# Performance work log

Measured on AMD Instinct MI355X. Metric: run time of the kernel, lower is better.

The kernel has to match this reference:

```python
import jax, jax.numpy as jnp
from jax import lax
import numpy as np

P, K1, K2 = 8, 5, 9  # nPaths, small/large ECA kernel sizes (from nDim=1024, nPaths=8)
LN_EPS = 1e-5


def setup_inputs() -> dict:
    key = jax.random.key(0)
    ks = jax.random.split(key, 6)
    b, c, l = 16, 1024, 4096
    return {
        "x": jax.random.normal(ks[0], (b, c, l), dtype=jnp.float32),
        "conv1_w": jax.random.normal(ks[1], (P, K1), dtype=jnp.float32) * 0.3,
        "conv2_w": jax.random.normal(ks[2], (P, K2), dtype=jnp.float32) * 0.3,
        "combine_w": jax.random.normal(ks[3], (2,), dtype=jnp.float32) * 0.5,
        "combine_b": jnp.zeros((), dtype=jnp.float32),
        "ln_g": jnp.ones((P,), dtype=jnp.float32),
        "ln_b": jnp.zeros((P,), dtype=jnp.float32),
        "W1": jax.random.normal(ks[4], (P, 2 * P), dtype=jnp.float32) * 0.3,
        "b1": jnp.zeros((2 * P,), dtype=jnp.float32),
        "W2": jax.random.normal(ks[5], (2 * P, P), dtype=jnp.float32) * 0.3,
        "b2": jnp.zeros((P,), dtype=jnp.float32),
    }


def _grouped_conv(y, w):
    # y: (b, P, D) pooled per-path features; w: (P, k) one 1-ch kernel per path.
    # Equivalent to the per-path Conv1d(1,1,k, padding=(k-1)//2) loop, fused.
    k = w.shape[-1]
    pad = (k - 1) // 2
    return lax.conv_general_dilated(
        y, w[:, None, :], window_strides=(1,), padding=[(pad, pad)],
        dimension_numbers=("NCH", "OIH", "NCH"), feature_group_count=y.shape[1])


def reference(x, conv1_w, conv2_w, combine_w, combine_b, ln_g, ln_b, W1, b1, W2, b2):
    b, c, l = x.shape
    nP = conv1_w.shape[0]
    D = c // nP
    pf = x.reshape(b, nP, D, l)          # (b, P, D, l)
    y = pf.mean(-1)                      # (b, P, D) global-avg-pool over l
    y1 = _grouped_conv(y, conv1_w)       # (b, P, D)
    y2 = _grouped_conv(y, conv2_w)       # (b, P, D)
    # combine = Conv1d(2,1,1): scalar mix of the two conv outputs + bias
    attn = jax.nn.sigmoid(combine_w[0] * y1 + combine_w[1] * y2 + combine_b)
    # cross-path gating MLP on per-path mean attention
    cross = attn.mean(-1)                # (b, P)
    mu = cross.mean(-1, keepdims=True)
    var = cross.var(-1, keepdims=True)   # biased, matches torch LayerNorm
    h = (cross - mu) / jnp.sqrt(var + LN_EPS) * ln_g + ln_b
    h = jax.nn.gelu(h @ W1 + b1, approximate=False)
    gate = jax.nn.sigmoid(h @ W2 + b2)   # (b, P)
    scale = attn * gate[:, :, None]      # (b, P, D)
    out = pf * scale[..., None]          # broadcast over l
    return out.reshape(b, c, l)
```

## Files before the change

### kernel.cpp

```cpp
#include <hip/hip_runtime.h>
#include <math.h>

#define NP 8
#define ND 128
#define NC 1024
#define NL 4096
#define NB 16
#define LN_EPS 1e-5f

#define NBLK 1024
#define NT   512
#define RPC  2
#define NCHUNK 8
#define GRPS 32

typedef float v4f __attribute__((ext_vector_type(4)));

__device__ __forceinline__ float hsum(v4f v) { return v.x + v.y + v.z + v.w; }
__device__ __forceinline__ float sigmoid_f(float z) { return 1.f / (1.f + expf(-z)); }

__device__ __forceinline__ float gelu_f(float s) {
    const float t = 0.7978845608028654f * (s + 0.044715f * s * s * s);
    const float e = expf(2.f * t);
    return 0.5f * s * (1.f + (e - 1.f) / (e + 1.f));
}

__global__ __launch_bounds__(NT, 8) void fused_kernel(
    const float* __restrict__ x, float* __restrict__ y,
    unsigned* __restrict__ garr, unsigned* __restrict__ grel,
    unsigned* __restrict__ root,
    const float* __restrict__ conv1_w, const float* __restrict__ conv2_w,
    const float* __restrict__ combine_w, const float* __restrict__ combine_b,
    const float* __restrict__ ln_g, const float* __restrict__ ln_b,
    const float* __restrict__ W1, const float* __restrict__ b1,
    const float* __restrict__ W2, const float* __restrict__ b2,
    float* __restrict__ out)
{
    const int tid  = threadIdx.x;
    const int bid  = blockIdx.x;
    const int grp  = bid >> 5;
    const bool lead = (bid & 31) == 0;
    const int r    = tid >> 8;
    const int col  = tid & 255;

    __shared__ v4f   srow[RPC][NL / 4];
    __shared__ float sy[NC];
    __shared__ float sred[RPC][4];
    __shared__ float scross[NP];
    __shared__ float sh[NP];
    __shared__ float sh2[2 * NP];
    __shared__ float sgate[NP];
    __shared__ float sml[2];
    __shared__ float sscale[RPC];

    for (int c = 0; c < NCHUNK; ++c) {
        const int r0  = c * (NBLK * RPC) + RPC * bid;
        const int b   = r0 >> 10;
        const int ch0 = r0 & (NC - 1);

        {
            const v4f* xr = (const v4f*)x + (size_t)(r0 + r) * (NL / 4);
            v4f v0 = xr[col], v1 = xr[col + 256], v2 = xr[col + 512], v3 = xr[col + 768];
            srow[r][col]       = v0;
            srow[r][col + 256] = v1;
            srow[r][col + 512] = v2;
            srow[r][col + 768] = v3;
            float ps = hsum(v0) + hsum(v1) + hsum(v2) + hsum(v3);
            ps += __shfl_down(ps, 32, 64); ps += __shfl_down(ps, 16, 64);
            ps += __shfl_down(ps, 8, 64);  ps += __shfl_down(ps, 4, 64);
            ps += __shfl_down(ps, 2, 64);  ps += __shfl_down(ps, 1, 64);
            if ((tid & 63) == 0) sred[r][(tid >> 6) & 3] = ps;
        }
        __syncthreads();
        if (tid == 0) {
            #pragma unroll
            for (int rr = 0; rr < RPC; ++rr) {
                const float ym = (sred[rr][0] + sred[rr][1] + sred[rr][2] + sred[rr][3]) * (1.f / NL);
                __hip_atomic_store(&y[r0 + rr], ym, __ATOMIC_RELAXED, __HIP_MEMORY_SCOPE_AGENT);
            }
            unsigned old = __hip_atomic_fetch_add(&garr[grp], 1u,
                              __ATOMIC_RELEASE, __HIP_MEMORY_SCOPE_AGENT);
            if (old == (unsigned)(c * 32 + 31))
                __hip_atomic_fetch_add(root, 1u,
                              __ATOMIC_RELEASE, __HIP_MEMORY_SCOPE_AGENT);
            if (lead) {
                while (__hip_atomic_load(root, __ATOMIC_RELAXED,
                                         __HIP_MEMORY_SCOPE_AGENT) < (unsigned)((c + 1) * GRPS))
                    __builtin_amdgcn_s_sleep(4);
                __hip_atomic_store(&grel[grp], (unsigned)(c + 1),
                                   __ATOMIC_RELAXED, __HIP_MEMORY_SCOPE_AGENT);
            } else {
                while (__hip_atomic_load(&grel[grp], __ATOMIC_RELAXED,
                                         __HIP_MEMORY_SCOPE_AGENT) < (unsigned)(c + 1))
                    __builtin_amdgcn_s_sleep(4);
            }
        }
        __syncthreads();

        {
            const float* yb = y + b * NC;
            sy[tid]       = __hip_atomic_load(&yb[tid],       __ATOMIC_RELAXED, __HIP_MEMORY_SCOPE_AGENT);
            sy[tid + 512] = __hip_atomic_load(&yb[tid + 512], __ATOMIC_RELAXED, __HIP_MEMORY_SCOPE_AGENT);
        }
        __syncthreads();
        float aa0, aa1;
        {
            #pragma unroll
            for (int k = 0; k < 2; ++k) {
                const int pos = 2 * tid + k;
                const int p = pos >> 7, d = pos & 127;
                const float* rowp = sy + p * ND;
                float c1 = 0.f;
                #pragma unroll
                for (int t = 0; t < 5; ++t) {
                    int dd = d + t - 2;
                    float v = (dd >= 0 && dd < ND) ? rowp[dd] : 0.f;
                    c1 += conv1_w[p * 5 + t] * v;
                }
                float c2 = 0.f;
                #pragma unroll
                for (int t = 0; t < 9; ++t) {
                    int dd = d + t - 4;
                    float v = (dd >= 0 && dd < ND) ? rowp[dd] : 0.f;
                    c2 += conv2_w[p * 9 + t] * v;
                }
                const float a = sigmoid_f(combine_w[0] * c1 + combine_w[1] * c2 + combine_b[0]);
                if (k == 0) aa0 = a; else aa1 = a;
            }
            float s = aa0 + aa1;
            s += __shfl_down(s, 32, 64); s += __shfl_down(s, 16, 64);
            s += __shfl_down(s, 8, 64);  s += __shfl_down(s, 4, 64);
            s += __shfl_down(s, 2, 64);  s += __shfl_down(s, 1, 64);
            if ((tid & 63) == 0) scross[tid >> 6] = s * (1.f / ND);
        }
        __syncthreads();
        if (tid == 0) {
            float mu = 0.f;
            #pragma unroll
            for (int pp = 0; pp < NP; ++pp) mu += scross[pp];
            mu *= (1.f / NP);
            float var = 0.f;
            #pragma unroll
            for (int pp = 0; pp < NP; ++pp) { float dl = scross[pp] - mu; var += dl * dl; }
            sml[0] = mu;
            sml[1] = rsqrtf(var * (1.f / NP) + LN_EPS);
        }
        __syncthreads();
        if (tid < NP)
            sh[tid] = (scross[tid] - sml[0]) * sml[1] * ln_g[tid] + ln_b[tid];
        __syncthreads();
        if (tid < 2 * NP) {
            float s = b1[tid];
            #pragma unroll
            for (int pp = 0; pp < NP; ++pp) s += sh[pp] * W1[pp * (2 * NP) + tid];
            sh2[tid] = gelu_f(s);
        }
        __syncthreads();
        if (tid < NP) {
            float s = b2[tid];
            #pragma unroll
            for (int j = 0; j < 2 * NP; ++j) s += sh2[j] * W2[j * NP + tid];
            sgate[tid] = sigmoid_f(s);
        }
        __syncthreads();
        if (tid == (ch0 >> 1)) {
            const float g = sgate[ch0 >> 7];
            sscale[0] = aa0 * g;
            sscale[1] = aa1 * g;
        }
        __syncthreads();

        {
            const float sc = sscale[r];
            v4f* orow = (v4f*)out + (size_t)(r0 + r) * (NL / 4);
            __builtin_nontemporal_store(srow[r][col]       * sc, &orow[col]);
            __builtin_nontemporal_store(srow[r][col + 256] * sc, &orow[col + 256]);
            __builtin_nontemporal_store(srow[r][col + 512] * sc, &orow[col + 512]);
            __builtin_nontemporal_store(srow[r][col + 768] * sc, &orow[col + 768]);
        }
        __syncthreads();
    }
}

__global__ __launch_bounds__(256) void pool_kernel(const float* __restrict__ x,
                                                   float* __restrict__ y) {
    const int wid  = threadIdx.x >> 6;
    const int lane = threadIdx.x & 63;
    const int row  = blockIdx.x * 4 + wid;
    const v4f* xr = (const v4f*)(x + (size_t)row * NL);
    float s = 0.f;
    #pragma unroll
    for (int i = 0; i < 16; ++i) {
        v4f v = xr[lane + i * 64];
        s += v.x + v.y + v.z + v.w;
    }
    #pragma unroll
    for (int off = 32; off; off >>= 1) s += __shfl_down(s, off, 64);
    if (lane == 0) y[row] = s * (1.f / NL);
}

__global__ __launch_bounds__(1024) void attn_kernel(
    const float* __restrict__ y,
    const float* __restrict__ conv1_w, const float* __restrict__ conv2_w,
    const float* __restrict__ combine_w, const float* __restrict__ combine_b,
    const float* __restrict__ ln_g, const float* __restrict__ ln_b,
    const float* __restrict__ W1, const float* __restrict__ b1,
    const float* __restrict__ W2, const float* __restrict__ b2,
    float* __restrict__ scale)
{
    const int b = blockIdx.x;
    const int tid = threadIdx.x;
    const int p = tid >> 7;
    const int d = tid & 127;

    __shared__ float sy[NC];
    __shared__ float sattn[NC];
    __shared__ float sred[16];
    __shared__ float scross[NP];
    __shared__ float sh[NP];
    __shared__ float sh2[2 * NP];
    __shared__ float sgate[NP];
    __shared__ float sml[2];

    sy[tid] = y[b * NC + tid];
    __syncthreads();

    const float* rowp = sy + p * ND;
    float c1 = 0.f;
    #pragma unroll
    for (int t = 0; t < 5; ++t) {
        int dd = d + t - 2;
        float v = (dd >= 0 && dd < ND) ? rowp[dd] : 0.f;
        c1 += conv1_w[p * 5 + t] * v;
    }
    float c2 = 0.f;
    #pragma unroll
    for (int t = 0; t < 9; ++t) {
        int dd = d + t - 4;
        float v = (dd >= 0 && dd < ND) ? rowp[dd] : 0.f;
        c2 += conv2_w[p * 9 + t] * v;
    }
    const float a = sigmoid_f(combine_w[0] * c1 + combine_w[1] * c2 + combine_b[0]);
    sattn[tid] = a;

    float rr = a;
    #pragma unroll
    for (int off = 32; off; off >>= 1) rr += __shfl_down(rr, off, 64);
    const int lane = tid & 63, wid = tid >> 6;
    if (lane == 0) sred[wid] = rr;
    __syncthreads();

    if (tid == 0) {
        float mu = 0.f, var = 0.f;
        #pragma unroll
        for (int pp = 0; pp < NP; ++pp) {
            scross[pp] = (sred[2 * pp] + sred[2 * pp + 1]) * (1.f / ND);
            mu += scross[pp];
        }
        mu *= (1.f / NP);
        #pragma unroll
        for (int pp = 0; pp < NP; ++pp) { float dl = scross[pp] - mu; var += dl * dl; }
        sml[0] = mu;
        sml[1] = rsqrtf(var * (1.f / NP) + LN_EPS);
    }
    __syncthreads();
    if (tid < NP)
        sh[tid] = (scross[tid] - sml[0]) * sml[1] * ln_g[tid] + ln_b[tid];
    __syncthreads();
    if (tid < 2 * NP) {
        float s = b1[tid];
        #pragma unroll
        for (int pp = 0; pp < NP; ++pp) s += sh[pp] * W1[pp * (2 * NP) + tid];
        sh2[tid] = gelu_f(s);
    }
    __syncthreads();
    if (tid < NP) {
        float s = b2[tid];
        #pragma unroll
        for (int j = 0; j < 2 * NP; ++j) s += sh2[j] * W2[j * NP + tid];
        sgate[tid] = sigmoid_f(s);
    }
    __syncthreads();

    scale[b * NC + tid] = sattn[tid] * sgate[p];
}

__global__ __launch_bounds__(256) void scale_kernel(const float* __restrict__ x,
                                                    const float* __restrict__ scale,
                                                    float* __restrict__ out) {
    const v4f* xv = (const v4f*)x;
    v4f* ov = (v4f*)out;
    const size_t n = (size_t)NB * NC * (NL / 4);
    const size_t stride = (size_t)gridDim.x * blockDim.x;
    for (size_t i = (size_t)blockIdx.x * blockDim.x + threadIdx.x; i < n; i += stride) {
        const float s = scale[i >> 10];
        v4f v = xv[i];
        v *= s;
        __builtin_nontemporal_store(v, &ov[i]);
    }
}

extern "C" void kernel_launch(void* const* d_in, const int* in_sizes, int n_in,
                              void* d_out, int out_size, void* d_ws, size_t ws_size,
                              hipStream_t stream) {
    const float* x         = (const float*)d_in[0];
    const float* conv1_w   = (const float*)d_in[1];
    const float* conv2_w   = (const float*)d_in[2];
    const float* combine_w = (const float*)d_in[3];
    const float* combine_b = (const float*)d_in[4];
    const float* ln_g      = (const float*)d_in[5];
    const float* ln_b      = (const float*)d_in[6];
    const float* W1        = (const float*)d_in[7];
    const float* b1        = (const float*)d_in[8];
    const float* W2        = (const float*)d_in[9];
    const float* b2        = (const float*)d_in[10];
    float* out = (float*)d_out;

    float* y        = (float*)d_ws;
    float* scale    = y + NB * NC;
    unsigned* garr  = (unsigned*)(void*)scale;
    unsigned* grel  = garr + GRPS;
    unsigned* root  = grel + GRPS;

    hipMemsetAsync((void*)garr, 0, (2 * GRPS + 16) * sizeof(unsigned), stream);

    int nb = 0;
    hipOccupancyMaxActiveBlocksPerMultiprocessor(&nb, fused_kernel, NT, 0);
    if (nb >= 4) {
        void* args[] = { (void*)&x, (void*)&y, (void*)&garr, (void*)&grel, (void*)&root,
                         (void*)&conv1_w, (void*)&conv2_w,
                         (void*)&combine_w, (void*)&combine_b,
                         (void*)&ln_g, (void*)&ln_b,
                         (void*)&W1, (void*)&b1, (void*)&W2, (void*)&b2,
                         (void*)&out };
        hipLaunchCooperativeKernel((const void*)fused_kernel, dim3(NBLK), dim3(NT),
                                   args, 0, stream);
    } else {
        pool_kernel<<<NB * NC / 4, 256, 0, stream>>>(x, y);
        attn_kernel<<<NB, 1024, 0, stream>>>(y, conv1_w, conv2_w, combine_w, combine_b,
                                             ln_g, ln_b, W1, b1, W2, b2, scale);
        scale_kernel<<<2048, 256, 0, stream>>>(x, scale, out);
    }
}
```

Measured before the change: 137.3 us.

## Software-pipeline fused kernel: overlap next row load with barrier wait and gating

```diff
diff --git a/kernel.cpp b/kernel.cpp
--- a/kernel.cpp
+++ b/kernel.cpp
@@ -10,8 +10,7 @@
 
 #define NBLK 1024
 #define NT   512
-#define RPC  2
-#define NCHUNK 8
+#define NCHUNK 16
 #define GRPS 32
 
 typedef float v4f __attribute__((ext_vector_type(4)));
@@ -25,7 +24,34 @@
     return 0.5f * s * (1.f + (e - 1.f) / (e + 1.f));
 }
 
-__global__ __launch_bounds__(NT, 8) void fused_kernel(
+__device__ __forceinline__ float attn_pos(const float* __restrict__ sy, int pos,
+                                          const float* __restrict__ c1w,
+                                          const float* __restrict__ c2w,
+                                          float w0, float w1, float cb) {
+    const int p = pos >> 7, d = pos & 127;
+    const float* rowp = sy + p * ND;
+    float c1 = 0.f;
+    #pragma unroll
+    for (int t = 0; t < 5; ++t) {
+        int dd = d + t - 2;
+        float v = (dd >= 0 && dd < ND) ? rowp[dd] : 0.f;
+        c1 += c1w[p * 5 + t] * v;
+    }
+    float c2 = 0.f;
+    #pragma unroll
+    for (int t = 0; t < 9; ++t) {
+        int dd = d + t - 4;
+        float v = (dd >= 0 && dd < ND) ? rowp[dd] : 0.f;
+        c2 += c2w[p * 9 + t] * v;
+    }
+    return sigmoid_f(w0 * c1 + w1 * c2 + cb);
+}
+
+#define WREDUCE(ps) { ps += __shfl_down(ps, 32, 64); ps += __shfl_down(ps, 16, 64); \
+    ps += __shfl_down(ps, 8, 64); ps += __shfl_down(ps, 4, 64); \
+    ps += __shfl_down(ps, 2, 64); ps += __shfl_down(ps, 1, 64); }
+
+__global__ __launch_bounds__(NT, 4) void fused_kernel(
     const float* __restrict__ x, float* __restrict__ y,
     unsigned* __restrict__ garr, unsigned* __restrict__ grel,
     unsigned* __restrict__ root,
@@ -40,145 +66,117 @@
     const int bid  = blockIdx.x;
     const int grp  = bid >> 5;
     const bool lead = (bid & 31) == 0;
-    const int r    = tid >> 8;
-    const int col  = tid & 255;
-
-    __shared__ v4f   srow[RPC][NL / 4];
+    const int pth  = bid >> 7;
+
+    __shared__ v4f   srow[2][NL / 4];
     __shared__ float sy[NC];
-    __shared__ float sred[RPC][4];
-    __shared__ float scross[NP];
-    __shared__ float sh[NP];
-    __shared__ float sh2[2 * NP];
-    __shared__ float sgate[NP];
-    __shared__ float sml[2];
-    __shared__ float sscale[RPC];
-
-    for (int c = 0; c < NCHUNK; ++c) {
-        const int r0  = c * (NBLK * RPC) + RPC * bid;
-        const int b   = r0 >> 10;
-        const int ch0 = r0 & (NC - 1);
-
-        {
-            const v4f* xr = (const v4f*)x + (size_t)(r0 + r) * (NL / 4);
-            v4f v0 = xr[col], v1 = xr[col + 256], v2 = xr[col + 512], v3 = xr[col + 768];
-            srow[r][col]       = v0;
-            srow[r][col + 256] = v1;
-            srow[r][col + 512] = v2;
-            srow[r][col + 768] = v3;
-            float ps = hsum(v0) + hsum(v1) + hsum(v2) + hsum(v3);
-            ps += __shfl_down(ps, 32, 64); ps += __shfl_down(ps, 16, 64);
-            ps += __shfl_down(ps, 8, 64);  ps += __shfl_down(ps, 4, 64);
-            ps += __shfl_down(ps, 2, 64);  ps += __shfl_down(ps, 1, 64);
-            if ((tid & 63) == 0) sred[r][(tid >> 6) & 3] = ps;
+    __shared__ float sredP[8];
+    __shared__ float sredA[8], sredB[8];
+    __shared__ float scross[NP], sh[NP], sh2[2 * NP], sgate[NP], sml[2];
+    __shared__ float sattn_own;
+    __shared__ float sscale[2];
+
+    for (int c = 0; c < NCHUNK + 2; ++c) {
+        if (c >= 2) {
+            const int rowp = (c - 2) * NBLK + bid;
+            const float sc = sscale[c & 1];
+            v4f* orow = (v4f*)out + (size_t)rowp * (NL / 4);
+            __builtin_nontemporal_store(srow[c & 1][tid]       * sc, &orow[tid]);
+            __builtin_nontemporal_store(srow[c & 1][tid + 512] * sc, &orow[tid + 512]);
         }
-        __syncthreads();
-        if (tid == 0) {
-            #pragma unroll
-            for (int rr = 0; rr < RPC; ++rr) {
-                const float ym = (sred[rr][0] + sred[rr][1] + sred[rr][2] + sred[rr][3]) * (1.f / NL);
-                __hip_atomic_store(&y[r0 + rr], ym, __ATOMIC_RELAXED, __HIP_MEMORY_SCOPE_AGENT);
-            }
-            unsigned old = __hip_atomic_fetch_add(&garr[grp], 1u,
-                              __ATOMIC_RELEASE, __HIP_MEMORY_SCOPE_AGENT);
-            if (old == (unsigned)(c * 32 + 31))
-                __hip_atomic_fetch_add(root, 1u,
-                              __ATOMIC_RELEASE, __HIP_MEMORY_SCOPE_AGENT);
-            if (lead) {
-                while (__hip_atomic_load(root, __ATOMIC_RELAXED,
-                                         __HIP_MEMORY_SCOPE_AGENT) < (unsigned)((c + 1) * GRPS))
-                    __builtin_amdgcn_s_sleep(4);
-                __hip_atomic_store(&grel[grp], (unsigned)(c + 1),
+
+        if (c < NCHUNK) {
+            const int rowc = c * NBLK + bid;
+            const v4f* xr = (const v4f*)x + (size_t)rowc * (NL / 4);
+            v4f v0 = xr[tid], v1 = xr[tid + 512];
+            srow[c & 1][tid]       = v0;
+            srow[c & 1][tid + 512] = v1;
+            float ps = hsum(v0) + hsum(v1);
+            WREDUCE(ps)
+            if ((tid & 63) == 0) sredP[tid >> 6] = ps;
+            __syncthreads();
+            if (tid == 0) {
+                float s = sredP[0] + sredP[1] + sredP[2] + sredP[3]
+                        + sredP[4] + sredP[5] + sredP[6] + sredP[7];
+                __hip_atomic_store(&y[rowc], s * (1.f / NL),
                                    __ATOMIC_RELAXED, __HIP_MEMORY_SCOPE_AGENT);
-            } else {
-                while (__hip_atomic_load(&grel[grp], __ATOMIC_RELAXED,
-                                         __HIP_MEMORY_SCOPE_AGENT) < (unsigned)(c + 1))
-                    __builtin_amdgcn_s_sleep(4);
+                unsigned old = __hip_atomic_fetch_add(&garr[grp], 1u,
+                                  __ATOMIC_RELEASE, __HIP_MEMORY_SCOPE_AGENT);
+                if (old == (unsigned)(c * 32 + 31))
+                    __hip_atomic_fetch_add(root, 1u,
+                                  __ATOMIC_RELEASE, __HIP_MEMORY_SCOPE_AGENT);
             }
         }
-        __syncthreads();
-
-        {
-            const float* yb = y + b * NC;
-            sy[tid]       = __hip_atomic_load(&yb[tid],       __ATOMIC_RELAXED, __HIP_MEMORY_SCOPE_AGENT);
-            sy[tid + 512] = __hip_atomic_load(&yb[tid + 512], __ATOMIC_RELAXED, __HIP_MEMORY_SCOPE_AGENT);
+
+        const int cb = c - 1;
+        if (cb >= 0 && cb < NCHUNK) {
+            if (tid == 0) {
+                if (lead) {
+                    while (__hip_atomic_load(root, __ATOMIC_ACQUIRE,
+                                             __HIP_MEMORY_SCOPE_AGENT) < (unsigned)((cb + 1) * GRPS))
+                        __builtin_amdgcn_s_sleep(2);
+                    __hip_atomic_store(&grel[grp], (unsigned)(cb + 1),
+                                       __ATOMIC_RELAXED, __HIP_MEMORY_SCOPE_AGENT);
+                } else {
+                    while (__hip_atomic_load(&grel[grp], __ATOMIC_RELAXED,
+                                             __HIP_MEMORY_SCOPE_AGENT) < (unsigned)(cb + 1))
+                        __builtin_amdgcn_s_sleep(2);
+                }
+            }
+            __syncthreads();
+            {
+                const float* yb = y + cb * NC;
+                sy[tid]       = __hip_atomic_load(&yb[tid],       __ATOMIC_RELAXED, __HIP_MEMORY_SCOPE_AGENT);
+                sy[tid + 512] = __hip_atomic_load(&yb[tid + 512], __ATOMIC_RELAXED, __HIP_MEMORY_SCOPE_AGENT);
+            }
+            __syncthreads();
+            const float w0 = combine_w[0], w1 = combine_w[1], cbb = combine_b[0];
+            float a0 = attn_pos(sy, tid,       conv1_w, conv2_w, w0, w1, cbb);
+            float a1 = attn_pos(sy, tid + 512, conv1_w, conv2_w, w0, w1, cbb);
+            if (tid == (bid & 511)) sattn_own = (bid < 512) ? a0 : a1;
+            float r0 = a0; WREDUCE(r0)
+            if ((tid & 63) == 0) sredA[tid >> 6] = r0;
+            float r1 = a1; WREDUCE(r1)
+            if ((tid & 63) == 0) sredB[tid >> 6] = r1;
+            __syncthreads();
+            if (tid < NP) {
+                float cr = (tid < 4) ? (sredA[2 * tid] + sredA[2 * tid + 1])
+                                     : (sredB[2 * (tid - 4)] + sredB[2 * (tid - 4) + 1]);
+                scross[tid] = cr * (1.f / ND);
+            }
+            __syncthreads();
+            if (tid == 0) {
+                float mu = 0.f;
+                #pragma unroll
+                for (int pp = 0; pp < NP; ++pp) mu += scross[pp];
+                mu *= (1.f / NP);
+                float var = 0.f;
+                #pragma unroll
+                for (int pp = 0; pp < NP; ++pp) { float dl = scross[pp] - mu; var += dl * dl; }
+                sml[0] = mu;
+                sml[1] = rsqrtf(var * (1.f / NP) + LN_EPS);
+            }
+            __syncthreads();
+            if (tid < NP)
+                sh[tid] = (scross[tid] - sml[0]) * sml[1] * ln_g[tid] + ln_b[tid];
+            __syncthreads();
+            if (tid < 2 * NP) {
+                float s = b1[tid];
+                #pragma unroll
+                for (int pp = 0; pp < NP; ++pp) s += sh[pp] * W1[pp * (2 * NP) + tid];
+                sh2[tid] = gelu_f(s);
+            }
+            __syncthreads();
+            if (tid < NP) {
+                float s = b2[tid];
+                #pragma unroll
+                for (int j = 0; j < 2 * NP; ++j) s += sh2[j] * W2[j * NP + tid];
+                sgate[tid] = sigmoid_f(s);
+            }
+            __syncthreads();
+            if (tid == 0) sscale[cb & 1] = sattn_own * sgate[pth];
+            __syncthreads();
         }
-        __syncthreads();
-        float aa0, aa1;
-        {
-            #pragma unroll
-            for (int k = 0; k < 2; ++k) {
-                const int pos = 2 * tid + k;
-                const int p = pos >> 7, d = pos & 127;
-                const float* rowp = sy + p * ND;
-                float c1 = 0.f;
-                #pragma unroll
-                for (int t = 0; t < 5; ++t) {
-                    int dd = d + t - 2;
-                    float v = (dd >= 0 && dd < ND) ? rowp[dd] : 0.f;
-                    c1 += conv1_w[p * 5 + t] * v;
-                }
-                float c2 = 0.f;
-                #pragma unroll
-                for (int t = 0; t < 9; ++t) {
-                    int dd = d + t - 4;
-                    float v = (dd >= 0 && dd < ND) ? rowp[dd] : 0.f;
-                    c2 += conv2_w[p * 9 + t] * v;
-                }
-                const float a = sigmoid_f(combine_w[0] * c1 + combine_w[1] * c2 + combine_b[0]);
-                if (k == 0) aa0 = a; else aa1 = a;
-            }
-            float s = aa0 + aa1;
-            s += __shfl_down(s, 32, 64); s += __shfl_down(s, 16, 64);
-            s += __shfl_down(s, 8, 64);  s += __shfl_down(s, 4, 64);
-            s += __shfl_down(s, 2, 64);  s += __shfl_down(s, 1, 64);
-            if ((tid & 63) == 0) scross[tid >> 6] = s * (1.f / ND);
-        }
-        __syncthreads();
-        if (tid == 0) {
-            float mu = 0.f;
-            #pragma unroll
-            for (int pp = 0; pp < NP; ++pp) mu += scross[pp];
-            mu *= (1.f / NP);
-            float var = 0.f;
-            #pragma unroll
-            for (int pp = 0; pp < NP; ++pp) { float dl = scross[pp] - mu; var += dl * dl; }
-            sml[0] = mu;
-            sml[1] = rsqrtf(var * (1.f / NP) + LN_EPS);
-        }
-        __syncthreads();
-        if (tid < NP)
-            sh[tid] = (scross[tid] - sml[0]) * sml[1] * ln_g[tid] + ln_b[tid];
-        __syncthreads();
-        if (tid < 2 * NP) {
-            float s = b1[tid];
-            #pragma unroll
-            for (int pp = 0; pp < NP; ++pp) s += sh[pp] * W1[pp * (2 * NP) + tid];
-            sh2[tid] = gelu_f(s);
-        }
-        __syncthreads();
-        if (tid < NP) {
-            float s = b2[tid];
-            #pragma unroll
-            for (int j = 0; j < 2 * NP; ++j) s += sh2[j] * W2[j * NP + tid];
-            sgate[tid] = sigmoid_f(s);
-        }
-        __syncthreads();
-        if (tid == (ch0 >> 1)) {
-            const float g = sgate[ch0 >> 7];
-            sscale[0] = aa0 * g;
-            sscale[1] = aa1 * g;
-        }
-        __syncthreads();
-
-        {
-            const float sc = sscale[r];
-            v4f* orow = (v4f*)out + (size_t)(r0 + r) * (NL / 4);
-            __builtin_nontemporal_store(srow[r][col]       * sc, &orow[col]);
-            __builtin_nontemporal_store(srow[r][col + 256] * sc, &orow[col + 256]);
-            __builtin_nontemporal_store(srow[r][col + 512] * sc, &orow[col + 512]);
-            __builtin_nontemporal_store(srow[r][col + 768] * sc, &orow[col + 768]);
-        }
-        __syncthreads();
     }
 }
 
```

Measured after the change: 137.7 us. No clear change (+0.3%).
